# Performance work log

Measured on AMD Instinct MI355X. Metric: run time of the kernel, lower is better.

## Reference

```python
import jax, jax.numpy as jnp
import numpy as np

H = 1024
N_HEADS = 16
DK = H // N_HEADS
B = 4
S_TGT = 1024
S_SRC = 1024
LN_EPS = 1e-5


def _ln(x, g, b):
    m = jnp.mean(x, axis=-1, keepdims=True)
    v = jnp.mean(jnp.square(x - m), axis=-1, keepdims=True)
    return (x - m) * jax.lax.rsqrt(v + LN_EPS) * g + b


def _mha(q_in, k_in, v_in, wq, wk, wv, wo, mask):
    # Equivalent to torch split(hidden//n_splits)+cat(dim=0) head layout:
    # per-(batch,head) scaled dot-product attention.
    Bq, Sq, _ = q_in.shape
    Sk = k_in.shape[1]
    q = (q_in @ wq).reshape(Bq, Sq, N_HEADS, DK)
    k = (k_in @ wk).reshape(Bq, Sk, N_HEADS, DK)
    v = (v_in @ wv).reshape(Bq, Sk, N_HEADS, DK)
    scores = jnp.einsum('bqhd,bkhd->bhqk', q, k)
    if mask is not None:
        scores = jnp.where(mask[:, None, :, :], -jnp.inf, scores)
    attn = jax.nn.softmax(scores / np.sqrt(DK).astype(np.float32), axis=-1)
    ctx = jnp.einsum('bhqk,bkhd->bqhd', attn, v).reshape(Bq, Sq, H)
    return ctx @ wo


def setup_inputs() -> dict:
    key = jax.random.key(0)
    ks = jax.random.split(key, 16)
    std = 1.0 / np.sqrt(H)
    p = {
        'x': jax.random.normal(ks[0], (B, S_TGT, H), jnp.float32),
        'key_and_value': jax.random.normal(ks[1], (B, S_SRC, H), jnp.float32),
        'mask': jnp.zeros((B, S_TGT, S_SRC), jnp.bool_),  # no padding
        # causal mask: True above the diagonal (masked positions)
        'future_mask': jnp.broadcast_to(
            jnp.triu(jnp.ones((S_TGT, S_TGT), jnp.bool_), k=1), (B, S_TGT, S_TGT)),
        'sa_wq': jax.random.normal(ks[2], (H, H), jnp.float32) * std,
        'sa_wk': jax.random.normal(ks[3], (H, H), jnp.float32) * std,
        'sa_wv': jax.random.normal(ks[4], (H, H), jnp.float32) * std,
        'sa_wo': jax.random.normal(ks[5], (H, H), jnp.float32) * std,
        'ca_wq': jax.random.normal(ks[6], (H, H), jnp.float32) * std,
        'ca_wk': jax.random.normal(ks[7], (H, H), jnp.float32) * std,
        'ca_wv': jax.random.normal(ks[8], (H, H), jnp.float32) * std,
        'ca_wo': jax.random.normal(ks[9], (H, H), jnp.float32) * std,
        'fc_w1': jax.random.normal(ks[10], (H, 4 * H), jnp.float32) * std,
        'fc_b1': jnp.zeros((4 * H,), jnp.float32),
        'fc_w2': jax.random.normal(ks[11], (4 * H, H), jnp.float32) * (0.5 * std),
        'fc_b2': jnp.zeros((H,), jnp.float32),
        'ln1_g': jnp.ones((H,), jnp.float32), 'ln1_b': jnp.zeros((H,), jnp.float32),
        'ln2_g': jnp.ones((H,), jnp.float32), 'ln2_b': jnp.zeros((H,), jnp.float32),
        'ln3_g': jnp.ones((H,), jnp.float32), 'ln3_b': jnp.zeros((H,), jnp.float32),
    }
    return p


def reference(x, key_and_value, mask, future_mask,
              sa_wq, sa_wk, sa_wv, sa_wo,
              ca_wq, ca_wk, ca_wv, ca_wo,
              fc_w1, fc_b1, fc_w2, fc_b2,
              ln1_g, ln1_b, ln2_g, ln2_b, ln3_g, ln3_b):
    # prev is None path (training); dropout in eval mode = identity.
    z = _ln(x, ln1_g, ln1_b)
    z = x + _mha(z, z, z, sa_wq, sa_wk, sa_wv, sa_wo, future_mask)
    nkv = _ln(key_and_value, ln2_g, ln2_b)
    z = z + _mha(_ln(z, ln2_g, ln2_b), nkv, nkv, ca_wq, ca_wk, ca_wv, ca_wo, mask)
    h = jax.nn.relu(_ln(z, ln3_g, ln3_b) @ fc_w1 + fc_b1)
    z = z + (h @ fc_w2 + fc_b2)
    return z
```

## Files before the change

kernel.cpp:

```cpp
#include <hip/hip_runtime.h>
#include <hip/hip_bf16.h>

typedef __attribute__((ext_vector_type(8))) short short8;
typedef __attribute__((ext_vector_type(4))) float f32x4;
using bf16 = __hip_bfloat16;

__device__ __forceinline__ void gload16(const void* g, void* l) {
  __builtin_amdgcn_global_load_lds(
      (const __attribute__((address_space(1))) void*)g,
      (__attribute__((address_space(3))) void*)l, 16, 0, 0);
}

__device__ __forceinline__ short f2bf(float f) {
  bf16 h = __float2bfloat16(f);
  short s;
  __builtin_memcpy(&s, &h, 2);
  return s;
}

__global__ __launch_bounds__(256)
void wtr8(const float* w0, const float* w1, const float* w2, const float* w3,
          const float* w4, const float* w5, const float* w6, const float* w7,
          bf16* __restrict__ Wout) {
  __shared__ float tile[32][33];
  const float* w;
  switch (blockIdx.z) {
    case 0: w = w0; break; case 1: w = w1; break;
    case 2: w = w2; break; case 3: w = w3; break;
    case 4: w = w4; break; case 5: w = w5; break;
    case 6: w = w6; break; default: w = w7; break;
  }
  bf16* wt = Wout + (size_t)blockIdx.z * 1024 * 1024;
  const int tx = threadIdx.x & 31, ty = threadIdx.x >> 5;
  const int c0 = blockIdx.x * 32, r0 = blockIdx.y * 32;
#pragma unroll
  for (int i = 0; i < 4; ++i)
    tile[ty * 4 + i][tx] = w[(size_t)(r0 + ty * 4 + i) * 1024 + c0 + tx];
  __syncthreads();
#pragma unroll
  for (int i = 0; i < 4; ++i) {
    const int cc = ty * 4 + i;
    wt[(size_t)(c0 + cc) * 1024 + r0 + tx] = __float2bfloat16(tile[tx][cc]);
  }
}

__global__ __launch_bounds__(256)
void wtr(const float* __restrict__ w, bf16* __restrict__ wt, int R, int C) {
  __shared__ float tile[32][33];
  const int tx = threadIdx.x & 31, ty = threadIdx.x >> 5;
  const int c0 = blockIdx.x * 32, r0 = blockIdx.y * 32;
#pragma unroll
  for (int i = 0; i < 4; ++i)
    tile[ty * 4 + i][tx] = w[(size_t)(r0 + ty * 4 + i) * C + c0 + tx];
  __syncthreads();
#pragma unroll
  for (int i = 0; i < 4; ++i) {
    const int cc = ty * 4 + i;
    wt[(size_t)(c0 + cc) * R + r0 + tx] = __float2bfloat16(tile[tx][cc]);
  }
}

__global__ __launch_bounds__(256)
void ln_k(const float* __restrict__ x, const float* __restrict__ g,
          const float* __restrict__ b, bf16* __restrict__ y) {
  const int row = blockIdx.x, t = threadIdx.x;
  const int wv = t >> 6, l = t & 63;
  const float4 v = reinterpret_cast<const float4*>(x + (size_t)row * 1024)[t];
  float s = v.x + v.y + v.z + v.w;
  float s2 = v.x * v.x + v.y * v.y + v.z * v.z + v.w * v.w;
#pragma unroll
  for (int m = 1; m < 64; m <<= 1) {
    s += __shfl_xor(s, m, 64);
    s2 += __shfl_xor(s2, m, 64);
  }
  __shared__ float ps[4], ps2[4];
  if (l == 0) { ps[wv] = s; ps2[wv] = s2; }
  __syncthreads();
  s = ps[0] + ps[1] + ps[2] + ps[3];
  s2 = ps2[0] + ps2[1] + ps2[2] + ps2[3];
  const float mean = s * (1.f / 1024.f);
  const float var = s2 * (1.f / 1024.f) - mean * mean;
  const float rs = rsqrtf(var + 1e-5f);
  const float4 gg = reinterpret_cast<const float4*>(g)[t];
  const float4 bb = reinterpret_cast<const float4*>(b)[t];
  ushort4 o;
  o.x = (unsigned short)f2bf((v.x - mean) * rs * gg.x + bb.x);
  o.y = (unsigned short)f2bf((v.y - mean) * rs * gg.y + bb.y);
  o.z = (unsigned short)f2bf((v.z - mean) * rs * gg.z + bb.z);
  o.w = (unsigned short)f2bf((v.w - mean) * rs * gg.w + bb.w);
  reinterpret_cast<ushort4*>(y + (size_t)row * 1024)[t] = o;
}

template <int BM, int EPI>
__global__ __launch_bounds__(256, 2)
void gemm_bt(const bf16* __restrict__ A, const bf16* __restrict__ BT,
             const float* bias, const float* res, void* outp,
             int M, int N, int K, bf16* vtp, int nv0) {
  constexpr int WM = BM / 32;
  constexpr int APASS = BM / 32;
  __shared__ alignas(16) short al[2][BM * 64];
  __shared__ alignas(16) short bl[2][128 * 64];
  const int t = threadIdx.x;
  const int gx = N >> 7;
  const int nwg = gridDim.x * gridDim.y;
  int id = blockIdx.y * gridDim.x + blockIdx.x;
  id = (id & 7) * (nwg >> 3) + (id >> 3);
  const int bx = id % gx, by = id / gx;
  const int m0 = by * BM, n0 = bx * 128;
  const int wv = t >> 6, l = t & 63, lr = l & 15, lk = l >> 4;
  const int wr = wv >> 1, wc = wv & 1;
  const int tr = t >> 3, tc = (t & 7) * 8;
  const int tcs = (((t & 7) ^ (tr & 7)) * 8);
  const int cro0 = ((lk ^ (lr & 7)) * 8);
  const int cro1 = (((4 + lk) ^ (lr & 7)) * 8);

  f32x4 acc[WM][4];
#pragma unroll
  for (int i = 0; i < WM; ++i)
#pragma unroll
    for (int j = 0; j < 4; ++j) acc[i][j] = (f32x4)0.f;

#define STAGE(buf, k0)                                                        \
  do {                                                                        \
    _Pragma("unroll") for (int it = 0; it < APASS; ++it) {                    \
      const int row = it * 32 + tr;                                           \
      gload16(A + (size_t)(m0 + row) * K + (k0) + tcs,                        \
              (char*)&al[buf][row * 64 + tc]);                                \
    }                                                                         \
    _Pragma("unroll") for (int it = 0; it < 4; ++it) {                        \
      const int row = it * 32 + tr;                                           \
      gload16(BT + (size_t)(n0 + row) * K + (k0) + tcs,                       \
              (char*)&bl[buf][row * 64 + tc]);                                \
    }                                                                         \
  } while (0)

#define COMPUTE(cur)                                                          \
  do {                                                                        \
    _Pragma("unroll") for (int ks = 0; ks < 2; ++ks) {                        \
      const int cro = ks ? cro1 : cro0;                                       \
      short8 af[WM], bfv[4];                                                  \
      _Pragma("unroll") for (int m = 0; m < WM; ++m) af[m] =                  \
          *reinterpret_cast<const short8*>(                                   \
              &al[cur][(wr * (BM / 2) + m * 16 + lr) * 64 + cro]);            \
      _Pragma("unroll") for (int n = 0; n < 4; ++n) bfv[n] =                  \
          *reinterpret_cast<const short8*>(                                   \
              &bl[cur][(wc * 64 + n * 16 + lr) * 64 + cro]);                  \
      _Pragma("unroll") for (int m = 0; m < WM; ++m)                          \
          _Pragma("unroll") for (int n = 0; n < 4; ++n) acc[m][n] =           \
              __builtin_amdgcn_mfma_f32_16x16x32_bf16(af[m], bfv[n],          \
                                                      acc[m][n], 0, 0, 0);    \
    }                                                                         \
  } while (0)

  const int nt = K >> 6;
  if constexpr (BM == 64) {
    STAGE(0, 0);
    STAGE(1, 64);
    for (int tk = 0; tk < nt; ++tk) {
      const int cur = tk & 1;
      if (tk < nt - 1)
        asm volatile("s_waitcnt vmcnt(6)" ::: "memory");
      else
        asm volatile("s_waitcnt vmcnt(0)" ::: "memory");
      __builtin_amdgcn_s_barrier();
      COMPUTE(cur);
      if (tk + 2 < nt) {
        asm volatile("s_waitcnt lgkmcnt(0)" ::: "memory");
        __builtin_amdgcn_s_barrier();
        STAGE(cur, (tk + 2) << 6);
      }
    }
  } else {
    STAGE(0, 0);
    asm volatile("s_waitcnt vmcnt(0)" ::: "memory");
    __syncthreads();
    for (int tk = 0; tk < nt; ++tk) {
      const int cur = tk & 1;
      if (tk + 1 < nt) STAGE(cur ^ 1, (tk + 1) << 6);
      COMPUTE(cur);
      asm volatile("s_waitcnt vmcnt(0)" ::: "memory");
      __syncthreads();
    }
  }
#undef STAGE
#undef COMPUTE

  const int r0 = m0 + wr * (BM / 2), c0 = n0 + wc * 64;
  if constexpr (EPI == 4) {
#pragma unroll
    for (int m = 0; m < WM; ++m) {
      const int rowb = r0 + m * 16 + lk * 4;
      const int bb = rowb >> 10, s0 = rowb & 1023;
#pragma unroll
      for (int n = 0; n < 4; ++n) {
        const int col = c0 + n * 16 + lr;
        if (col < nv0) {
#pragma unroll
          for (int r = 0; r < 4; ++r)
            ((bf16*)outp)[(size_t)(rowb + r) * nv0 + col] =
                __float2bfloat16(acc[m][n][r]);
        } else {
          ushort4 u;
          u.x = (unsigned short)f2bf(acc[m][n][0]);
          u.y = (unsigned short)f2bf(acc[m][n][1]);
          u.z = (unsigned short)f2bf(acc[m][n][2]);
          u.w = (unsigned short)f2bf(acc[m][n][3]);
          const size_t vidx = ((size_t)bb * 1024 + (col - nv0)) * 1024 + s0;
          *reinterpret_cast<ushort4*>(vtp + vidx) = u;
        }
      }
    }
  } else {
#pragma unroll
    for (int m = 0; m < WM; ++m)
#pragma unroll
      for (int n = 0; n < 4; ++n) {
        const int col = c0 + n * 16 + lr;
#pragma unroll
        for (int r = 0; r < 4; ++r) {
          const int row = r0 + m * 16 + lk * 4 + r;
          const size_t idx = (size_t)row * N + col;
          float v = acc[m][n][r];
          if (EPI == 0) {
            ((bf16*)outp)[idx] = __float2bfloat16(v);
          } else if (EPI == 1) {
            ((float*)outp)[idx] = res[idx] + v;
          } else if (EPI == 2) {
            v += bias[col];
            ((bf16*)outp)[idx] = __float2bfloat16(fmaxf(v, 0.f));
          } else {
            ((float*)outp)[idx] = res[idx] + v + bias[col];
          }
        }
      }
  }
}

template <int EPI>
__global__ __launch_bounds__(512, 1)
void gemm256(const bf16* __restrict__ A, const bf16* __restrict__ BT,
             const float* __restrict__ bias, void* __restrict__ outp,
             int M, int N, int K, bf16* vtp, int nv0) {
  __shared__ alignas(16) short al[2][256 * 64];
  __shared__ alignas(16) short bl[2][256 * 64];
  const int t = threadIdx.x;
  const int gx = N >> 8;
  const int nwg = gridDim.x * gridDim.y;
  int id = blockIdx.y * gridDim.x + blockIdx.x;
  id = (id & 7) * (nwg >> 3) + (id >> 3);
  const int bx = id % gx, by = id / gx;
  const int m0 = by * 256, n0 = bx * 256;
  const int wid = t >> 6, l = t & 63, lr = l & 15, lk = l >> 4;
  const int wm = wid >> 2, wn = wid & 3;
  const int tr = t >> 3, tc = (t & 7) * 8;
  const int tcs = (((t & 7) ^ (tr & 7)) * 8);
  const int cro0 = ((lk ^ (lr & 7)) * 8);
  const int cro1 = (((4 + lk) ^ (lr & 7)) * 8);

  f32x4 acc[8][4];
#pragma unroll
  for (int i = 0; i < 8; ++i)
#pragma unroll
    for (int j = 0; j < 4; ++j) acc[i][j] = (f32x4)0.f;

#define STAGE2(buf, k0)                                                       \
  do {                                                                        \
    _Pragma("unroll") for (int it = 0; it < 4; ++it) {                        \
      const int row = it * 64 + tr;                                           \
      gload16(A + (size_t)(m0 + row) * K + (k0) + tcs,                        \
              (char*)&al[buf][row * 64 + tc]);                                \
    }                                                                         \
    _Pragma("unroll") for (int it = 0; it < 4; ++it) {                        \
      const int row = it * 64 + tr;                                           \
      gload16(BT + (size_t)(n0 + row) * K + (k0) + tcs,                       \
              (char*)&bl[buf][row * 64 + tc]);                                \
    }                                                                         \
  } while (0)

#define COMPUTE2(cur)                                                         \
  do {                                                                        \
    _Pragma("unroll") for (int ks = 0; ks < 2; ++ks) {                        \
      const int cro = ks ? cro1 : cro0;                                       \
      short8 af[8], bfv[4];                                                   \
      _Pragma("unroll") for (int m = 0; m < 8; ++m) af[m] =                   \
          *reinterpret_cast<const short8*>(                                   \
              &al[cur][(wm * 128 + m * 16 + lr) * 64 + cro]);                 \
      _Pragma("unroll") for (int n = 0; n < 4; ++n) bfv[n] =                  \
          *reinterpret_cast<const short8*>(                                   \
              &bl[cur][(wn * 64 + n * 16 + lr) * 64 + cro]);                  \
      _Pragma("unroll") for (int m = 0; m < 8; ++m)                           \
          _Pragma("unroll") for (int n = 0; n < 4; ++n) acc[m][n] =           \
              __builtin_amdgcn_mfma_f32_16x16x32_bf16(af[m], bfv[n],          \
                                                      acc[m][n], 0, 0, 0);    \
    }                                                                         \
  } while (0)

  const int nt = K >> 6;
  STAGE2(0, 0);
  STAGE2(1, 64);
  for (int tk = 0; tk < nt; ++tk) {
    const int cur = tk & 1;
    if (tk < nt - 1)
      asm volatile("s_waitcnt vmcnt(8)" ::: "memory");
    else
      asm volatile("s_waitcnt vmcnt(0)" ::: "memory");
    __builtin_amdgcn_s_barrier();
    COMPUTE2(cur);
    if (tk + 2 < nt) {
      asm volatile("s_waitcnt lgkmcnt(0)" ::: "memory");
      __builtin_amdgcn_s_barrier();
      STAGE2(cur, (tk + 2) << 6);
    }
  }
#undef STAGE2
#undef COMPUTE2

  const int r0 = m0 + wm * 128, c0 = n0 + wn * 64;
  if constexpr (EPI == 2) {
#pragma unroll
    for (int m = 0; m < 8; ++m)
#pragma unroll
      for (int n = 0; n < 4; ++n) {
        const int col = c0 + n * 16 + lr;
        const float bcol = bias[col];
#pragma unroll
        for (int r = 0; r < 4; ++r) {
          const int row = r0 + m * 16 + lk * 4 + r;
          const float v = acc[m][n][r] + bcol;
          ((bf16*)outp)[(size_t)row * N + col] =
              __float2bfloat16(fmaxf(v, 0.f));
        }
      }
  } else {
#pragma unroll
    for (int m = 0; m < 8; ++m) {
      const int rowb = r0 + m * 16 + lk * 4;
      const int bb = rowb >> 10, s0 = rowb & 1023;
#pragma unroll
      for (int n = 0; n < 4; ++n) {
        const int col = c0 + n * 16 + lr;
        if (col < nv0) {
#pragma unroll
          for (int r = 0; r < 4; ++r)
            ((bf16*)outp)[(size_t)(rowb + r) * nv0 + col] =
                __float2bfloat16(acc[m][n][r]);
        } else {
          ushort4 u;
          u.x = (unsigned short)f2bf(acc[m][n][0]);
          u.y = (unsigned short)f2bf(acc[m][n][1]);
          u.z = (unsigned short)f2bf(acc[m][n][2]);
          u.w = (unsigned short)f2bf(acc[m][n][3]);
          const size_t vidx = ((size_t)bb * 1024 + (col - nv0)) * 1024 + s0;
          *reinterpret_cast<ushort4*>(vtp + vidx) = u;
        }
      }
    }
  }
}

template <bool CAUSAL>
__global__ __launch_bounds__(256, 2)
void flash8(const bf16* __restrict__ Qb, int ldq,
            const bf16* __restrict__ Kb, int ldk,
            const bf16* __restrict__ VTb, bf16* __restrict__ Ob) {
  __shared__ alignas(16) short kl[3][64 * 64];
  __shared__ alignas(16) short vl[3][64 * 64];
  __shared__ alignas(16) short pl[4][32 * 72];
  const int t = threadIdx.x, wv = t >> 6, l = t & 63, lr = l & 15, lk = l >> 4;
  const int raw = blockIdx.y * 8 + blockIdx.x;
  const int id = (raw & 7) * 64 + (raw >> 3);
  const int qb = id & 7, bh = id >> 3;
  const int b = bh >> 4, h = bh & 15;
  const size_t rowbase = (size_t)b * 1024;
  const int q0 = qb * 128 + wv * 32;
  const bf16* Vbase = VTb + (rowbase + h * 64) * 1024;

  const int tr = t >> 3;
  const int tcd = (t & 7) * 8;
  const int tcs = (((t & 7) ^ (tr & 7)) * 8);
  const int cro0 = ((lk ^ (lr & 7)) * 8);
  const int cro1 = (((4 + lk) ^ (lr & 7)) * 8);

  short8 qf[2][2];
#pragma unroll
  for (int m = 0; m < 2; ++m)
#pragma unroll
    for (int ks = 0; ks < 2; ++ks)
      qf[m][ks] = *reinterpret_cast<const short8*>(
          Qb + (rowbase + q0 + m * 16 + lr) * ldq + h * 64 + ks * 32 + lk * 8);

  short8 ones;
#pragma unroll
  for (int j = 0; j < 8; ++j) ones[j] = (short)0x3F80;

  f32x4 accO[2][4];
  f32x4 accL[2];
#pragma unroll
  for (int m = 0; m < 2; ++m) {
#pragma unroll
    for (int n = 0; n < 4; ++n) accO[m][n] = (f32x4)0.f;
    accL[m] = (f32x4)0.f;
  }

  const int ntb = CAUSAL ? (qb * 2 + 2) : 16;
  const int myLast = q0 >> 6;

#define FSTAGE(buf, kv0)                                                      \
  do {                                                                        \
    _Pragma("unroll") for (int it = 0; it < 2; ++it) {                        \
      const int row = it * 32 + tr;                                           \
      gload16(Kb + (rowbase + (kv0) + row) * ldk + h * 64 + tcs,              \
              (char*)&kl[buf][row * 64 + tcd]);                               \
    }                                                                         \
    _Pragma("unroll") for (int it = 0; it < 2; ++it) {                        \
      const int row = it * 32 + tr;                                           \
      gload16(Vbase + (size_t)row * 1024 + (kv0) + tcs,                       \
              (char*)&vl[buf][row * 64 + tcd]);                               \
    }                                                                         \
  } while (0)

  FSTAGE(0, 0);
  FSTAGE(1, 64);
  int cur = 0;
  for (int tk = 0; tk < ntb; ++tk) {
    if (tk < ntb - 1)
      asm volatile("s_waitcnt vmcnt(4)" ::: "memory");
    else
      asm volatile("s_waitcnt vmcnt(0)" ::: "memory");
    __builtin_amdgcn_s_barrier();
    if (tk + 2 < ntb) {
      int stg = cur + 2;
      if (stg >= 3) stg -= 3;
      FSTAGE(stg, (tk + 2) << 6);
    }
    if (!CAUSAL || tk <= myLast) {
      const int kv0 = tk * 64;
      const bool needmask = CAUSAL && (tk == myLast);
      f32x4 sa[2][4];
#pragma unroll
      for (int m = 0; m < 2; ++m)
#pragma unroll
        for (int n = 0; n < 4; ++n) sa[m][n] = (f32x4)0.f;
#pragma unroll
      for (int ks = 0; ks < 2; ++ks) {
        const int cro = ks ? cro1 : cro0;
        short8 kf[4];
#pragma unroll
        for (int n = 0; n < 4; ++n)
          kf[n] = *reinterpret_cast<const short8*>(
              &kl[cur][(n * 16 + lr) * 64 + cro]);
        __builtin_amdgcn_s_setprio(1);
#pragma unroll
        for (int m = 0; m < 2; ++m)
#pragma unroll
          for (int n = 0; n < 4; ++n)
            sa[m][n] = __builtin_amdgcn_mfma_f32_16x16x32_bf16(
                qf[m][ks], kf[n], sa[m][n], 0, 0, 0);
        __builtin_amdgcn_s_setprio(0);
      }
#pragma unroll
      for (int m = 0; m < 2; ++m) {
#pragma unroll
        for (int r = 0; r < 4; ++r) {
          const int row = q0 + m * 16 + lk * 4 + r;
          float s0 = sa[m][0][r] * 0.125f, s1 = sa[m][1][r] * 0.125f;
          float s2 = sa[m][2][r] * 0.125f, s3 = sa[m][3][r] * 0.125f;
          if (needmask) {
            if (kv0 + 0 + lr > row) s0 = -1e30f;
            if (kv0 + 16 + lr > row) s1 = -1e30f;
            if (kv0 + 32 + lr > row) s2 = -1e30f;
            if (kv0 + 48 + lr > row) s3 = -1e30f;
          }
          const float p0 = __expf(s0), p1 = __expf(s1);
          const float p2 = __expf(s2), p3 = __expf(s3);
          const int prow = m * 16 + lk * 4 + r;
          pl[wv][prow * 72 + lr + 0] = f2bf(p0);
          pl[wv][prow * 72 + lr + 16] = f2bf(p1);
          pl[wv][prow * 72 + lr + 32] = f2bf(p2);
          pl[wv][prow * 72 + lr + 48] = f2bf(p3);
        }
      }
#pragma unroll
      for (int ks = 0; ks < 2; ++ks) {
        const int cro = ks ? cro1 : cro0;
        short8 pf[2], vf[4];
#pragma unroll
        for (int m = 0; m < 2; ++m)
          pf[m] = *reinterpret_cast<const short8*>(
              &pl[wv][(m * 16 + lr) * 72 + ks * 32 + lk * 8]);
#pragma unroll
        for (int n = 0; n < 4; ++n)
          vf[n] = *reinterpret_cast<const short8*>(
              &vl[cur][(n * 16 + lr) * 64 + cro]);
        __builtin_amdgcn_s_setprio(1);
#pragma unroll
        for (int m = 0; m < 2; ++m) {
#pragma unroll
          for (int n = 0; n < 4; ++n)
            accO[m][n] = __builtin_amdgcn_mfma_f32_16x16x32_bf16(
                pf[m], vf[n], accO[m][n], 0, 0, 0);
          accL[m] = __builtin_amdgcn_mfma_f32_16x16x32_bf16(
              pf[m], ones, accL[m], 0, 0, 0);
        }
        __builtin_amdgcn_s_setprio(0);
      }
    }
    cur = (cur + 1 == 3) ? 0 : cur + 1;
  }
#undef FSTAGE

#pragma unroll
  for (int m = 0; m < 2; ++m)
#pragma unroll
    for (int n = 0; n < 4; ++n)
#pragma unroll
      for (int r = 0; r < 4; ++r) {
        const int row = q0 + m * 16 + lk * 4 + r;
        const int col = n * 16 + lr;
        const float o = accO[m][n][r] / accL[m][r];
        Ob[(rowbase + row) * 1024 + h * 64 + col] = __float2bfloat16(o);
      }
}

extern "C" void kernel_launch(void* const* d_in, const int* in_sizes, int n_in,
                              void* d_out, int out_size, void* d_ws,
                              size_t ws_size, hipStream_t stream) {
  const float* x = (const float*)d_in[0];
  const float* kv_in = (const float*)d_in[1];
  const float* sa_wq = (const float*)d_in[4];
  const float* sa_wk = (const float*)d_in[5];
  const float* sa_wv = (const float*)d_in[6];
  const float* sa_wo = (const float*)d_in[7];
  const float* ca_wq = (const float*)d_in[8];
  const float* ca_wk = (const float*)d_in[9];
  const float* ca_wv = (const float*)d_in[10];
  const float* ca_wo = (const float*)d_in[11];
  const float* fc_w1 = (const float*)d_in[12];
  const float* fc_b1 = (const float*)d_in[13];
  const float* fc_w2 = (const float*)d_in[14];
  const float* fc_b2 = (const float*)d_in[15];
  const float* ln1_g = (const float*)d_in[16];
  const float* ln1_b = (const float*)d_in[17];
  const float* ln2_g = (const float*)d_in[18];
  const float* ln2_b = (const float*)d_in[19];
  const float* ln3_g = (const float*)d_in[20];
  const float* ln3_b = (const float*)d_in[21];

  char* ws = (char*)d_ws;
  const size_t MB = 1024 * 1024;
  bf16* W = (bf16*)ws;
  bf16* w1T = W + 8 * MB;
  bf16* w2T = W + 12 * MB;
  float* z = (float*)(ws + 32 * MB);
  bf16* t0 = (bf16*)(ws + 48 * MB);
  bf16* qkvb = (bf16*)(ws + 56 * MB);
  bf16* vts = (bf16*)(ws + 72 * MB);
  bf16* kb = (bf16*)(ws + 80 * MB);
  bf16* vtc = (bf16*)(ws + 88 * MB);
  bf16* qb = (bf16*)(ws + 96 * MB);
  bf16* ctx = (bf16*)(ws + 104 * MB);
  bf16* kvln = (bf16*)(ws + 112 * MB);
  bf16* hb = (bf16*)(ws + 120 * MB);

  const dim3 B256(256);
  wtr8<<<dim3(32, 32, 8), B256, 0, stream>>>(sa_wq, sa_wk, sa_wv, sa_wo,
                                             ca_wq, ca_wk, ca_wv, ca_wo, W);
  wtr<<<dim3(128, 32), B256, 0, stream>>>(fc_w1, w1T, 1024, 4096);
  wtr<<<dim3(32, 128), B256, 0, stream>>>(fc_w2, w2T, 4096, 1024);

  ln_k<<<4096, B256, 0, stream>>>(x, ln1_g, ln1_b, t0);
  gemm256<4><<<dim3(12, 16), dim3(512), 0, stream>>>(
      t0, W, nullptr, qkvb, 4096, 3072, 1024, vts, 2048);
  flash8<true><<<dim3(8, 64), B256, 0, stream>>>(
      qkvb, 2048, qkvb + 1024, 2048, vts, ctx);
  gemm_bt<64, 1><<<dim3(8, 64), B256, 0, stream>>>(
      ctx, W + 3 * MB, nullptr, x, z, 4096, 1024, 1024, nullptr, 0);

  ln_k<<<4096, B256, 0, stream>>>(kv_in, ln2_g, ln2_b, kvln);
  ln_k<<<4096, B256, 0, stream>>>(z, ln2_g, ln2_b, t0);
  gemm256<4><<<dim3(8, 16), dim3(512), 0, stream>>>(
      kvln, W + 5 * MB, nullptr, kb, 4096, 2048, 1024, vtc, 1024);
  gemm_bt<64, 0><<<dim3(8, 64), B256, 0, stream>>>(
      t0, W + 4 * MB, nullptr, nullptr, qb, 4096, 1024, 1024, nullptr, 0);
  flash8<false><<<dim3(8, 64), B256, 0, stream>>>(
      qb, 1024, kb, 1024, vtc, ctx);
  gemm_bt<64, 1><<<dim3(8, 64), B256, 0, stream>>>(
      ctx, W + 7 * MB, nullptr, z, z, 4096, 1024, 1024, nullptr, 0);

  ln_k<<<4096, B256, 0, stream>>>(z, ln3_g, ln3_b, t0);
  gemm256<2><<<dim3(16, 16), dim3(512), 0, stream>>>(
      t0, w1T, fc_b1, hb, 4096, 4096, 1024, nullptr, 0);
  gemm_bt<64, 3><<<dim3(8, 64), B256, 0, stream>>>(
      hb, w2T, fc_b2, z, d_out, 4096, 1024, 4096, nullptr, 0);
}
```

Baseline: 348.2 us.

## Fuse self-attn QKV and cross-attn KV projections into one dual GEMM launch

Adds a gemm256_dual kernel that runs the self-attention QKV projection and the cross-attention KV projection in a single 320-workgroup launch, choosing operands by block id. The key/value LayerNorm is moved earlier so both inputs are ready. The goal is to fill more CUs and cut one launch plus the tail idle time of two under-filled grids. The remaining gemm256 is specialised to the bias+ReLU epilogue. The combined grid of 1.25 waves may still leave a partial tail.

```diff
diff --git a/kernel.cpp b/kernel.cpp
--- a/kernel.cpp
+++ b/kernel.cpp
@@ -236,11 +236,10 @@
   }
 }
 
-template <int EPI>
 __global__ __launch_bounds__(512, 1)
 void gemm256(const bf16* __restrict__ A, const bf16* __restrict__ BT,
-             const float* __restrict__ bias, void* __restrict__ outp,
-             int M, int N, int K, bf16* vtp, int nv0) {
+             const float* __restrict__ bias, bf16* __restrict__ outp,
+             int M, int N, int K) {
   __shared__ alignas(16) short al[2][256 * 64];
   __shared__ alignas(16) short bl[2][256 * 64];
   const int t = threadIdx.x;
@@ -312,47 +311,133 @@
       STAGE2(cur, (tk + 2) << 6);
     }
   }
+
+  const int r0 = m0 + wm * 128, c0 = n0 + wn * 64;
+#pragma unroll
+  for (int m = 0; m < 8; ++m)
+#pragma unroll
+    for (int n = 0; n < 4; ++n) {
+      const int col = c0 + n * 16 + lr;
+      const float bcol = bias[col];
+#pragma unroll
+      for (int r = 0; r < 4; ++r) {
+        const int row = r0 + m * 16 + lk * 4 + r;
+        const float v = acc[m][n][r] + bcol;
+        outp[(size_t)row * N + col] = __float2bfloat16(fmaxf(v, 0.f));
+      }
+    }
 #undef STAGE2
 #undef COMPUTE2
+}
+
+__global__ __launch_bounds__(512, 1)
+void gemm256_dual(const bf16* __restrict__ A0, const bf16* __restrict__ BT0,
+                  bf16* __restrict__ out0, bf16* __restrict__ vt0,
+                  const bf16* __restrict__ A1, const bf16* __restrict__ BT1,
+                  bf16* __restrict__ out1, bf16* __restrict__ vt1) {
+  __shared__ alignas(16) short al[2][256 * 64];
+  __shared__ alignas(16) short bl[2][256 * 64];
+  const int t = threadIdx.x;
+  const int raw = blockIdx.x;
+  const int id = (raw & 7) * 40 + (raw >> 3);
+  const bf16 *A, *BT;
+  bf16 *outp, *vtp;
+  int nv0, gx, pid;
+  if (id < 192) {
+    A = A0; BT = BT0; outp = out0; vtp = vt0; nv0 = 2048; gx = 12; pid = id;
+  } else {
+    A = A1; BT = BT1; outp = out1; vtp = vt1; nv0 = 1024; gx = 8;
+    pid = id - 192;
+  }
+  const int K = 1024;
+  const int bx = pid % gx, by = pid / gx;
+  const int m0 = by * 256, n0 = bx * 256;
+  const int wid = t >> 6, l = t & 63, lr = l & 15, lk = l >> 4;
+  const int wm = wid >> 2, wn = wid & 3;
+  const int tr = t >> 3, tc = (t & 7) * 8;
+  const int tcs = (((t & 7) ^ (tr & 7)) * 8);
+  const int cro0 = ((lk ^ (lr & 7)) * 8);
+  const int cro1 = (((4 + lk) ^ (lr & 7)) * 8);
+
+  f32x4 acc[8][4];
+#pragma unroll
+  for (int i = 0; i < 8; ++i)
+#pragma unroll
+    for (int j = 0; j < 4; ++j) acc[i][j] = (f32x4)0.f;
+
+#define STAGE2(buf, k0)                                                       \
+  do {                                                                        \
+    _Pragma("unroll") for (int it = 0; it < 4; ++it) {                        \
+      const int row = it * 64 + tr;                                           \
+      gload16(A + (size_t)(m0 + row) * K + (k0) + tcs,                        \
+              (char*)&al[buf][row * 64 + tc]);                                \
+    }                                                                         \
+    _Pragma("unroll") for (int it = 0; it < 4; ++it) {                        \
+      const int row = it * 64 + tr;                                           \
+      gload16(BT + (size_t)(n0 + row) * K + (k0) + tcs,                       \
+              (char*)&bl[buf][row * 64 + tc]);                                \
+    }                                                                         \
+  } while (0)
+
+#define COMPUTE2(cur)                                                         \
+  do {                                                                        \
+    _Pragma("unroll") for (int ks = 0; ks < 2; ++ks) {                        \
+      const int cro = ks ? cro1 : cro0;                                       \
+      short8 af[8], bfv[4];                                                   \
+      _Pragma("unroll") for (int m = 0; m < 8; ++m) af[m] =                   \
+          *reinterpret_cast<const short8*>(                                   \
+              &al[cur][(wm * 128 + m * 16 + lr) * 64 + cro]);                 \
+      _Pragma("unroll") for (int n = 0; n < 4; ++n) bfv[n] =                  \
+          *reinterpret_cast<const short8*>(                                   \
+              &bl[cur][(wn * 64 + n * 16 + lr) * 64 + cro]);                  \
+      _Pragma("unroll") for (int m = 0; m < 8; ++m)                           \
+          _Pragma("unroll") for (int n = 0; n < 4; ++n) acc[m][n] =           \
+              __builtin_amdgcn_mfma_f32_16x16x32_bf16(af[m], bfv[n],          \
+                                                      acc[m][n], 0, 0, 0);    \
+    }                                                                         \
+  } while (0)
+
+  const int nt = K >> 6;
+  STAGE2(0, 0);
+  STAGE2(1, 64);
+  for (int tk = 0; tk < nt; ++tk) {
+    const int cur = tk & 1;
+    if (tk < nt - 1)
+      asm volatile("s_waitcnt vmcnt(8)" ::: "memory");
+    else
+      asm volatile("s_waitcnt vmcnt(0)" ::: "memory");
+    __builtin_amdgcn_s_barrier();
+    COMPUTE2(cur);
+    if (tk + 2 < nt) {
+      asm volatile("s_waitcnt lgkmcnt(0)" ::: "memory");
+      __builtin_amdgcn_s_barrier();
+      STAGE2(cur, (tk + 2) << 6);
+    }
+  }
+#undef STAGE2
+#undef COMPUTE2
 
   const int r0 = m0 + wm * 128, c0 = n0 + wn * 64;
-  if constexpr (EPI == 2) {
-#pragma unroll
-    for (int m = 0; m < 8; ++m)
-#pragma unroll
-      for (int n = 0; n < 4; ++n) {
-        const int col = c0 + n * 16 + lr;
-        const float bcol = bias[col];
-#pragma unroll
-        for (int r = 0; r < 4; ++r) {
-          const int row = r0 + m * 16 + lk * 4 + r;
-          const float v = acc[m][n][r] + bcol;
-          ((bf16*)outp)[(size_t)row * N + col] =
-              __float2bfloat16(fmaxf(v, 0.f));
-        }
-      }
-  } else {
-#pragma unroll
-    for (int m = 0; m < 8; ++m) {
-      const int rowb = r0 + m * 16 + lk * 4;
-      const int bb = rowb >> 10, s0 = rowb & 1023;
-#pragma unroll
-      for (int n = 0; n < 4; ++n) {
-        const int col = c0 + n * 16 + lr;
-        if (col < nv0) {
-#pragma unroll
-          for (int r = 0; r < 4; ++r)
-            ((bf16*)outp)[(size_t)(rowb + r) * nv0 + col] =
-                __float2bfloat16(acc[m][n][r]);
-        } else {
-          ushort4 u;
-          u.x = (unsigned short)f2bf(acc[m][n][0]);
-          u.y = (unsigned short)f2bf(acc[m][n][1]);
-          u.z = (unsigned short)f2bf(acc[m][n][2]);
-          u.w = (unsigned short)f2bf(acc[m][n][3]);
-          const size_t vidx = ((size_t)bb * 1024 + (col - nv0)) * 1024 + s0;
-          *reinterpret_cast<ushort4*>(vtp + vidx) = u;
-        }
+#pragma unroll
+  for (int m = 0; m < 8; ++m) {
+    const int rowb = r0 + m * 16 + lk * 4;
+    const int bb = rowb >> 10, s0 = rowb & 1023;
+#pragma unroll
+    for (int n = 0; n < 4; ++n) {
+      const int col = c0 + n * 16 + lr;
+      if (col < nv0) {
+#pragma unroll
+        for (int r = 0; r < 4; ++r)
+          outp[(size_t)(rowb + r) * nv0 + col] =
+              __float2bfloat16(acc[m][n][r]);
+      } else {
+        ushort4 u;
+        u.x = (unsigned short)f2bf(acc[m][n][0]);
+        u.y = (unsigned short)f2bf(acc[m][n][1]);
+        u.z = (unsigned short)f2bf(acc[m][n][2]);
+        u.w = (unsigned short)f2bf(acc[m][n][3]);
+        const size_t vidx = ((size_t)bb * 1024 + (col - nv0)) * 1024 + s0;
+        *reinterpret_cast<ushort4*>(vtp + vidx) = u;
       }
     }
   }
@@ -569,17 +654,16 @@
   wtr<<<dim3(32, 128), B256, 0, stream>>>(fc_w2, w2T, 4096, 1024);
 
   ln_k<<<4096, B256, 0, stream>>>(x, ln1_g, ln1_b, t0);
-  gemm256<4><<<dim3(12, 16), dim3(512), 0, stream>>>(
-      t0, W, nullptr, qkvb, 4096, 3072, 1024, vts, 2048);
+  ln_k<<<4096, B256, 0, stream>>>(kv_in, ln2_g, ln2_b, kvln);
+  gemm256_dual<<<dim3(320), dim3(512), 0, stream>>>(
+      t0, W, qkvb, vts, kvln, W + 5 * MB, kb, vtc);
+
   flash8<true><<<dim3(8, 64), B256, 0, stream>>>(
       qkvb, 2048, qkvb + 1024, 2048, vts, ctx);
   gemm_bt<64, 1><<<dim3(8, 64), B256, 0, stream>>>(
       ctx, W + 3 * MB, nullptr, x, z, 4096, 1024, 1024, nullptr, 0);
 
-  ln_k<<<4096, B256, 0, stream>>>(kv_in, ln2_g, ln2_b, kvln);
   ln_k<<<4096, B256, 0, stream>>>(z, ln2_g, ln2_b, t0);
-  gemm256<4><<<dim3(8, 16), dim3(512), 0, stream>>>(
-      kvln, W + 5 * MB, nullptr, kb, 4096, 2048, 1024, vtc, 1024);
   gemm_bt<64, 0><<<dim3(8, 64), B256, 0, stream>>>(
       t0, W + 4 * MB, nullptr, nullptr, qb, 4096, 1024, 1024, nullptr, 0);
   flash8<false><<<dim3(8, 64), B256, 0, stream>>>(
@@ -588,8 +672,8 @@
       ctx, W + 7 * MB, nullptr, z, z, 4096, 1024, 1024, nullptr, 0);
 
   ln_k<<<4096, B256, 0, stream>>>(z, ln3_g, ln3_b, t0);
-  gemm256<2><<<dim3(16, 16), dim3(512), 0, stream>>>(
-      t0, w1T, fc_b1, hb, 4096, 4096, 1024, nullptr, 0);
+  gemm256<<<dim3(16, 16), dim3(512), 0, stream>>>(
+      t0, w1T, fc_b1, hb, 4096, 4096, 1024);
   gemm_bt<64, 3><<<dim3(8, 64), B256, 0, stream>>>(
       hb, w2T, fc_b2, z, d_out, 4096, 1024, 4096, nullptr, 0);
 }
```

Result: faster. 333.2 us (-4.3%).
